# Kernel optimization log

Measured on AMD Instinct MI355X. Metric: run time of the kernel, lower is better.

The kernel has to match this reference:

```python
import jax, jax.numpy as jnp
import numpy as np

EMBED_DIM = 1024
NUM_HEADS = 16
HEAD_DIM = EMBED_DIM // NUM_HEADS
INV_SQRT_DIM = 1.0 / np.sqrt(EMBED_DIM).astype(np.float32)  # note: embed_dim, not head_dim


def setup_inputs() -> dict:
    key = jax.random.key(0)
    k1, k2 = jax.random.split(key)
    hidden_states = jax.random.normal(k1, (2, 2048, EMBED_DIM), dtype=jnp.float32)
    # nn.Linear(embed_dim, 3*embed_dim, bias=False); store as [in, out] so y = x @ w_qkv
    w_qkv = jax.random.normal(k2, (EMBED_DIM, 3 * EMBED_DIM), dtype=jnp.float32) * 0.02
    return {"hidden_states": hidden_states, "w_qkv": w_qkv}


def reference(hidden_states, w_qkv):
    b, s, _ = hidden_states.shape
    qkv = hidden_states @ w_qkv  # [b, s, 3*E]
    q, k, v = jnp.split(qkv, 3, axis=-1)

    def split_heads(x):  # [b, s, E] -> [b, h, s, d]
        return x.reshape(b, s, NUM_HEADS, HEAD_DIM).transpose(0, 2, 1, 3)

    q, k, v = split_heads(q), split_heads(k), split_heads(v)
    scores = jnp.einsum('bhqd,bhkd->bhqk', q, k) * INV_SQRT_DIM
    w = jax.nn.softmax(scores, axis=-1)
    out = jnp.einsum('bhqk,bhkd->bhqd', w, v)  # [b, h, s, d]
    return out.transpose(0, 2, 1, 3).reshape(b, s, EMBED_DIM)
```

## Files before the change

### kernel.cpp

```cpp
#include <hip/hip_runtime.h>
#include <stdint.h>


typedef __attribute__((ext_vector_type(8))) short v8s;
typedef __attribute__((ext_vector_type(4))) float v4f;
typedef __attribute__((ext_vector_type(16))) float f32x16;

__device__ __forceinline__ unsigned short bf16bits(float f) {
  union { float f; unsigned int u; } c; c.f = f;
  unsigned int u = c.u;
  unsigned int r = (u + 0x7fffu + ((u >> 16) & 1u)) >> 16;
  return (unsigned short)r;
}

__device__ __forceinline__ v4f mfma16(v8s a, v8s b, v4f c) {
  return __builtin_amdgcn_mfma_f32_16x16x32_bf16(a, b, c, 0, 0, 0);
}
__device__ __forceinline__ f32x16 mfma32(v8s a, v8s b, f32x16 c) {
  return __builtin_amdgcn_mfma_f32_32x32x16_bf16(a, b, c, 0, 0, 0);
}
__device__ __forceinline__ f32x16 zero16() {
  f32x16 z;
#pragma unroll
  for (int i = 0; i < 16; ++i) z[i] = 0.f;
  return z;
}
__device__ __forceinline__ unsigned int cvtpk(float lo, float hi) {
  unsigned int r;
  asm("v_cvt_pk_bf16_f32 %0, %1, %2" : "=v"(r) : "v"(lo), "v"(hi));
  return r;
}
__device__ __forceinline__ void pl32swap(unsigned int& a, unsigned int& b) {
  asm volatile("v_permlane32_swap_b32 %0, %1" : "+v"(a), "+v"(b));
}

#define GLD16(g, l) __builtin_amdgcn_global_load_lds( \
    (const __attribute__((address_space(1))) unsigned int*)(g), \
    (__attribute__((address_space(3))) unsigned int*)(l), 16, 0, 0)

__global__ __launch_bounds__(256) void cvt_x_kernel(const float4* __restrict__ x4,
                                                    ushort4* __restrict__ o4, int n4) {
  int i = blockIdx.x * 256 + threadIdx.x;
  if (i < n4) {
    float4 v = x4[i];
    ushort4 o;
    o.x = bf16bits(v.x); o.y = bf16bits(v.y); o.z = bf16bits(v.z); o.w = bf16bits(v.w);
    o4[i] = o;
  }
}

__global__ __launch_bounds__(256) void cvt_wT_kernel(const float* __restrict__ w,
                                                     unsigned short* __restrict__ wt) {
  __shared__ float t[32][33];
  int n0 = blockIdx.x * 32, k0 = blockIdx.y * 32;
  int tx = threadIdx.x & 31, ty = threadIdx.x >> 5;
  for (int i = 0; i < 4; ++i) {
    int kr = ty + i * 8;
    t[kr][tx] = w[(k0 + kr) * 3072 + n0 + tx];
  }
  __syncthreads();
  for (int i = 0; i < 4; ++i) {
    int nr = ty + i * 8;
    wt[(n0 + nr) * 1024 + k0 + tx] = bf16bits(t[tx][nr]);
  }
}

__global__ __launch_bounds__(256) void qkv_gemm(const unsigned short* __restrict__ A,
                                                const unsigned short* __restrict__ Bm,
                                                unsigned short* __restrict__ Cq,
                                                unsigned short* __restrict__ VTh) {
  __shared__ __align__(16) unsigned short S[24576];
  int bm = blockIdx.x, bn = blockIdx.y;
  int tid = threadIdx.x, lane = tid & 63, wave = tid >> 6;
  int wr = wave >> 1, wc = wave & 1;

  v4f acc[2][4];
  for (int i = 0; i < 2; ++i)
    for (int j = 0; j < 4; ++j) acc[i][j] = (v4f){0.f, 0.f, 0.f, 0.f};

  auto STAGE = [&](int hh, int kk) {
    unsigned short* As = S + hh * 12288;
    unsigned short* Bs = As + 4096;
    for (int i = 0; i < 2; ++i) {
      int e = i * 256 + tid;
      int row = e >> 3, cc = e & 7;
      int sc = cc ^ (row & 7);
      GLD16(A + (bm * 64 + row) * 1024 + kk + sc * 8,
            (char*)As + (i * 256 + wave * 64) * 16);
    }
    for (int i = 0; i < 4; ++i) {
      int e = i * 256 + tid;
      int row = e >> 3, cc = e & 7;
      int sc = cc ^ (row & 7);
      GLD16(Bm + (bn * 128 + row) * 1024 + kk + sc * 8,
            (char*)Bs + (i * 256 + wave * 64) * 16);
    }
  };
  auto COMPUTE = [&](int hh) {
    const unsigned short* As = S + hh * 12288;
    const unsigned short* Bs = As + 4096;
    for (int ks = 0; ks < 2; ++ks) {
      v8s af[2], bf[4];
      for (int rt = 0; rt < 2; ++rt) {
        int ra = wr * 32 + rt * 16 + (lane & 15);
        int ca = (ks * 4 + (lane >> 4)) ^ (ra & 7);
        af[rt] = *(const v8s*)&As[ra * 64 + ca * 8];
      }
      for (int ct = 0; ct < 4; ++ct) {
        int rb = wc * 64 + ct * 16 + (lane & 15);
        int cb = (ks * 4 + (lane >> 4)) ^ (rb & 7);
        bf[ct] = *(const v8s*)&Bs[rb * 64 + cb * 8];
      }
      for (int rt = 0; rt < 2; ++rt)
        for (int ct = 0; ct < 4; ++ct)
          acc[rt][ct] = mfma16(af[rt], bf[ct], acc[rt][ct]);
    }
  };

  STAGE(0, 0);
  __syncthreads();
  for (int kt = 0; kt < 15; ++kt) {
    STAGE((kt + 1) & 1, (kt + 1) * 64);
    COMPUTE(kt & 1);
    __syncthreads();
  }
  COMPUTE(1);
  __syncthreads();

  if (bn < 16) {
    float qs = (bn < 8) ? 0.0450842200f : 1.0f;
    for (int ct = 0; ct < 4; ++ct) {
      int col = wc * 64 + ct * 16 + (lane & 15);
      for (int rt = 0; rt < 2; ++rt)
        for (int j = 0; j < 4; ++j) {
          int m = wr * 32 + rt * 16 + ((lane >> 4) << 2) + j;
          S[m * 128 + (((col >> 3) ^ (m & 7)) << 3) + (col & 7)] =
              bf16bits(acc[rt][ct][j] * qs);
        }
    }
    __syncthreads();
    for (int i = 0; i < 4; ++i) {
      int c = i * 256 + tid;
      int m = c >> 4, c8 = c & 15;
      v8s v = *(const v8s*)&S[m * 128 + ((c8 ^ (m & 7)) << 3)];
      *(v8s*)&Cq[(size_t)(bm * 64 + m) * 2048 + bn * 128 + c8 * 8] = v;
    }
  } else {
    for (int ct = 0; ct < 4; ++ct) {
      int n = wc * 64 + ct * 16 + (lane & 15);
      for (int rt = 0; rt < 2; ++rt) {
        int m0 = wr * 32 + rt * 16 + ((lane >> 4) << 2);
        ushort4 p4;
        p4.x = bf16bits(acc[rt][ct][0]); p4.y = bf16bits(acc[rt][ct][1]);
        p4.z = bf16bits(acc[rt][ct][2]); p4.w = bf16bits(acc[rt][ct][3]);
        *(ushort4*)&S[n * 64 + (((m0 >> 3) ^ (n & 7)) << 3) + (m0 & 7)] = p4;
      }
    }
    __syncthreads();
    int b = bm >> 5, s0 = (bm & 31) * 64;
    for (int i = 0; i < 4; ++i) {
      int c = i * 256 + tid;
      int n = c >> 3, c8 = c & 7;
      v8s v = *(const v8s*)&S[n * 64 + ((c8 ^ (n & 7)) << 3)];
      int nn = bn * 128 + n - 2048;
      int head = nn >> 6, d = nn & 63;
      *(v8s*)&VTh[(size_t)((b * 16 + head) * 64 + d) * 2048 + s0 + c8 * 8] = v;
    }
  }
}

__global__ __launch_bounds__(256) void attn_kernel(const unsigned short* __restrict__ Cq,
                                                   const unsigned short* __restrict__ VTh,
                                                   float* __restrict__ out) {
  __shared__ __align__(16) unsigned short Qs[128 * 64];
  __shared__ __align__(16) unsigned short Ks[64 * 64];
  __shared__ __align__(16) unsigned short Vs[64 * 64];
  int tid = threadIdx.x, lane = tid & 63, wave = tid >> 6;
  int ln31 = lane & 31, h = lane >> 5;
  int wq = wave * 32;
  int flat = blockIdx.x + (blockIdx.y << 4);
  int swz = (flat & 7) * 64 + (flat >> 3);
  int qb = swz & 15, bh = swz >> 4;
  int b = bh >> 4, hH = bh & 15;

  const unsigned short* Qg = Cq + (size_t)(b * 2048 + qb * 128) * 2048 + hH * 64;
  const unsigned short* Kg = Cq + (size_t)(b * 2048) * 2048 + 1024 + hH * 64;
  const unsigned short* Vg = VTh + (size_t)bh * 64 * 2048;

  for (int i = 0; i < 4; ++i) {
    int e = i * 256 + tid;
    int row = e >> 3, cc = e & 7;
    int sc = cc ^ (row & 7);
    GLD16(Qg + (size_t)row * 2048 + sc * 8, (char*)Qs + (i * 256 + wave * 64) * 16);
  }
  __syncthreads();

  v8s qf[4];
#pragma unroll
  for (int ks = 0; ks < 4; ++ks) {
    int rq = wq + ln31;
    int cq = (ks * 2 + h) ^ (rq & 7);
    qf[ks] = *(const v8s*)&Qs[rq * 64 + cq * 8];
  }

  f32x16 acc0 = zero16(), acc1 = zero16();
  float rsum = 0.f;

  for (int kt = 0; kt < 32; ++kt) {
    __syncthreads();
    for (int i = 0; i < 2; ++i) {
      int e = i * 256 + tid;
      int row = e >> 3, cc = e & 7;
      int sc = cc ^ (row & 7);
      GLD16(Kg + (size_t)(kt * 64 + row) * 2048 + sc * 8,
            (char*)Ks + (i * 256 + wave * 64) * 16);
    }
    for (int i = 0; i < 2; ++i) {
      int e = i * 256 + tid;
      int row = e >> 3, cc = e & 7;
      int sc = cc ^ (row & 7);
      GLD16(Vg + row * 2048 + kt * 64 + sc * 8, (char*)Vs + (i * 256 + wave * 64) * 16);
    }
    __syncthreads();

    f32x16 s0 = zero16(), s1 = zero16();
#pragma unroll
    for (int ks = 0; ks < 4; ++ks) {
      int ck = (ks * 2 + h) ^ (ln31 & 7);
      v8s kf0 = *(const v8s*)&Ks[ln31 * 64 + ck * 8];
      v8s kf1 = *(const v8s*)&Ks[(32 + ln31) * 64 + ck * 8];
      s0 = mfma32(kf0, qf[ks], s0);
      s1 = mfma32(kf1, qf[ks], s1);
    }

#pragma unroll
    for (int mt = 0; mt < 2; ++mt) {
      const f32x16 st = mt ? s1 : s0;
      float p[16];
#pragma unroll
      for (int r = 0; r < 16; ++r) { p[r] = __builtin_amdgcn_exp2f(st[r]); rsum += p[r]; }
      unsigned int w0 = cvtpk(p[0], p[1]),  w1 = cvtpk(p[2], p[3]);
      unsigned int w2 = cvtpk(p[4], p[5]),  w3 = cvtpk(p[6], p[7]);
      unsigned int w4 = cvtpk(p[8], p[9]),  w5 = cvtpk(p[10], p[11]);
      unsigned int w6 = cvtpk(p[12], p[13]), w7 = cvtpk(p[14], p[15]);
      pl32swap(w0, w2); pl32swap(w1, w3);
      pl32swap(w4, w6); pl32swap(w5, w7);
      union { unsigned int u[4]; v8s v; } pa0, pa1;
      pa0.u[0] = w0; pa0.u[1] = w1; pa0.u[2] = w2; pa0.u[3] = w3;
      pa1.u[0] = w4; pa1.u[1] = w5; pa1.u[2] = w6; pa1.u[3] = w7;
#pragma unroll
      for (int s = 0; s < 2; ++s) {
        v8s pa = s ? pa1.v : pa0.v;
        int cb = mt * 4 + s * 2 + h;
        int rv0 = ln31, rv1 = 32 + ln31;
        v8s vb0 = *(const v8s*)&Vs[rv0 * 64 + ((cb ^ (rv0 & 7))) * 8];
        v8s vb1 = *(const v8s*)&Vs[rv1 * 64 + ((cb ^ (rv1 & 7))) * 8];
        acc0 = mfma32(pa, vb0, acc0);
        acc1 = mfma32(pa, vb1, acc1);
      }
    }
  }

  float rtot = rsum + __shfl_xor(rsum, 32, 64);
  float inv = 1.0f / rtot;

  int qbase = qb * 128 + wq;
#pragma unroll
  for (int r = 0; r < 16; ++r) {
    int qr = (r & 3) + 8 * (r >> 2) + 4 * h;
    float ivr = __shfl(inv, qr, 64);
    size_t o = (size_t)(b * 2048 + qbase + qr) * 1024 + hH * 64 + ln31;
    out[o] = acc0[r] * ivr;
    out[o + 32] = acc1[r] * ivr;
  }
}

extern "C" void kernel_launch(void* const* d_in, const int* in_sizes, int n_in,
                              void* d_out, int out_size, void* d_ws, size_t ws_size,
                              hipStream_t stream) {
  const float* x = (const float*)d_in[0];
  const float* w = (const float*)d_in[1];
  float* out = (float*)d_out;

  char* ws = (char*)d_ws;
  unsigned short* xb = (unsigned short*)ws;
  unsigned short* wT = (unsigned short*)(ws + 8388608);
  unsigned short* Cq = (unsigned short*)(ws + 14680064);
  unsigned short* VT = (unsigned short*)(ws + 31457280);

  cvt_x_kernel<<<4096, 256, 0, stream>>>((const float4*)x, (ushort4*)xb, 1048576);
  cvt_wT_kernel<<<dim3(96, 32), 256, 0, stream>>>(w, wT);
  qkv_gemm<<<dim3(64, 24), 256, 0, stream>>>(xb, wT, Cq, VT);
  attn_kernel<<<dim3(16, 32), 256, 0, stream>>>(Cq, VT, out);
}
```

Baseline: 156.2 us.

## Split attention KV loop across wave pairs and swizzle QKV GEMM block order

```diff
diff --git a/kernel.cpp b/kernel.cpp
--- a/kernel.cpp
+++ b/kernel.cpp
@@ -70,9 +70,11 @@
                                                 unsigned short* __restrict__ Cq,
                                                 unsigned short* __restrict__ VTh) {
   __shared__ __align__(16) unsigned short S[24576];
-  int bm = blockIdx.x, bn = blockIdx.y;
   int tid = threadIdx.x, lane = tid & 63, wave = tid >> 6;
   int wr = wave >> 1, wc = wave & 1;
+  int flat = blockIdx.x + blockIdx.y * 64;
+  int x = flat & 7, k = flat >> 3;
+  int bm = k & 63, bn = (k >> 6) * 8 + x;
 
   v4f acc[2][4];
   for (int i = 0; i < 2; ++i)
@@ -172,22 +174,22 @@
 __global__ __launch_bounds__(256) void attn_kernel(const unsigned short* __restrict__ Cq,
                                                    const unsigned short* __restrict__ VTh,
                                                    float* __restrict__ out) {
-  __shared__ __align__(16) unsigned short Qs[128 * 64];
-  __shared__ __align__(16) unsigned short Ks[64 * 64];
-  __shared__ __align__(16) unsigned short Vs[64 * 64];
+  __shared__ __align__(16) unsigned short Qs[64 * 64];
+  __shared__ __align__(16) unsigned short Ks[2][64 * 64];
+  __shared__ __align__(16) unsigned short Vs[2][64 * 64];
   int tid = threadIdx.x, lane = tid & 63, wave = tid >> 6;
   int ln31 = lane & 31, h = lane >> 5;
-  int wq = wave * 32;
-  int flat = blockIdx.x + (blockIdx.y << 4);
-  int swz = (flat & 7) * 64 + (flat >> 3);
-  int qb = swz & 15, bh = swz >> 4;
+  int qhalf = wave & 1, kpar = wave >> 1;
+  int flat = blockIdx.x + (blockIdx.y << 5);
+  int swz = (flat & 7) * 128 + (flat >> 3);
+  int qb = swz & 31, bh = swz >> 5;
   int b = bh >> 4, hH = bh & 15;
 
-  const unsigned short* Qg = Cq + (size_t)(b * 2048 + qb * 128) * 2048 + hH * 64;
+  const unsigned short* Qg = Cq + (size_t)(b * 2048 + qb * 64) * 2048 + hH * 64;
   const unsigned short* Kg = Cq + (size_t)(b * 2048) * 2048 + 1024 + hH * 64;
   const unsigned short* Vg = VTh + (size_t)bh * 64 * 2048;
 
-  for (int i = 0; i < 4; ++i) {
+  for (int i = 0; i < 2; ++i) {
     int e = i * 256 + tid;
     int row = e >> 3, cc = e & 7;
     int sc = cc ^ (row & 7);
@@ -198,7 +200,7 @@
   v8s qf[4];
 #pragma unroll
   for (int ks = 0; ks < 4; ++ks) {
-    int rq = wq + ln31;
+    int rq = qhalf * 32 + ln31;
     int cq = (ks * 2 + h) ^ (rq & 7);
     qf[ks] = *(const v8s*)&Qs[rq * 64 + cq * 8];
   }
@@ -206,29 +208,32 @@
   f32x16 acc0 = zero16(), acc1 = zero16();
   float rsum = 0.f;
 
-  for (int kt = 0; kt < 32; ++kt) {
+  for (int t = 0; t < 16; ++t) {
     __syncthreads();
     for (int i = 0; i < 2; ++i) {
       int e = i * 256 + tid;
       int row = e >> 3, cc = e & 7;
       int sc = cc ^ (row & 7);
-      GLD16(Kg + (size_t)(kt * 64 + row) * 2048 + sc * 8,
-            (char*)Ks + (i * 256 + wave * 64) * 16);
-    }
-    for (int i = 0; i < 2; ++i) {
-      int e = i * 256 + tid;
-      int row = e >> 3, cc = e & 7;
-      int sc = cc ^ (row & 7);
-      GLD16(Vg + row * 2048 + kt * 64 + sc * 8, (char*)Vs + (i * 256 + wave * 64) * 16);
-    }
-    __syncthreads();
+      GLD16(Kg + (size_t)((2 * t) * 64 + row) * 2048 + sc * 8,
+            (char*)Ks[0] + (i * 256 + wave * 64) * 16);
+      GLD16(Kg + (size_t)((2 * t + 1) * 64 + row) * 2048 + sc * 8,
+            (char*)Ks[1] + (i * 256 + wave * 64) * 16);
+      GLD16(Vg + row * 2048 + (2 * t) * 64 + sc * 8,
+            (char*)Vs[0] + (i * 256 + wave * 64) * 16);
+      GLD16(Vg + row * 2048 + (2 * t + 1) * 64 + sc * 8,
+            (char*)Vs[1] + (i * 256 + wave * 64) * 16);
+    }
+    __syncthreads();
+
+    const unsigned short* Ksp = Ks[kpar];
+    const unsigned short* Vsp = Vs[kpar];
 
     f32x16 s0 = zero16(), s1 = zero16();
 #pragma unroll
     for (int ks = 0; ks < 4; ++ks) {
       int ck = (ks * 2 + h) ^ (ln31 & 7);
-      v8s kf0 = *(const v8s*)&Ks[ln31 * 64 + ck * 8];
-      v8s kf1 = *(const v8s*)&Ks[(32 + ln31) * 64 + ck * 8];
+      v8s kf0 = *(const v8s*)&Ksp[ln31 * 64 + ck * 8];
+      v8s kf1 = *(const v8s*)&Ksp[(32 + ln31) * 64 + ck * 8];
       s0 = mfma32(kf0, qf[ks], s0);
       s1 = mfma32(kf1, qf[ks], s1);
     }
@@ -253,25 +258,48 @@
         v8s pa = s ? pa1.v : pa0.v;
         int cb = mt * 4 + s * 2 + h;
         int rv0 = ln31, rv1 = 32 + ln31;
-        v8s vb0 = *(const v8s*)&Vs[rv0 * 64 + ((cb ^ (rv0 & 7))) * 8];
-        v8s vb1 = *(const v8s*)&Vs[rv1 * 64 + ((cb ^ (rv1 & 7))) * 8];
+        v8s vb0 = *(const v8s*)&Vsp[rv0 * 64 + ((cb ^ (rv0 & 7))) * 8];
+        v8s vb1 = *(const v8s*)&Vsp[rv1 * 64 + ((cb ^ (rv1 & 7))) * 8];
         acc0 = mfma32(pa, vb0, acc0);
         acc1 = mfma32(pa, vb1, acc1);
       }
     }
   }
 
-  float rtot = rsum + __shfl_xor(rsum, 32, 64);
-  float inv = 1.0f / rtot;
-
-  int qbase = qb * 128 + wq;
-#pragma unroll
-  for (int r = 0; r < 16; ++r) {
-    int qr = (r & 3) + 8 * (r >> 2) + 4 * h;
-    float ivr = __shfl(inv, qr, 64);
-    size_t o = (size_t)(b * 2048 + qbase + qr) * 1024 + hH * 64 + ln31;
-    out[o] = acc0[r] * ivr;
-    out[o + 32] = acc1[r] * ivr;
+  __syncthreads();
+  float* accx = (float*)&Ks[0][0];
+  float* rsx = (float*)&Vs[0][0];
+  if (kpar == 1) {
+    int r = qhalf;
+#pragma unroll
+    for (int j = 0; j < 16; ++j) {
+      accx[r * 2048 + j * 64 + lane] = acc0[j];
+      accx[r * 2048 + (16 + j) * 64 + lane] = acc1[j];
+    }
+    rsx[r * 64 + lane] = rsum;
+  }
+  __syncthreads();
+  if (kpar == 0) {
+    int r = qhalf;
+#pragma unroll
+    for (int j = 0; j < 16; ++j) {
+      acc0[j] += accx[r * 2048 + j * 64 + lane];
+      acc1[j] += accx[r * 2048 + (16 + j) * 64 + lane];
+    }
+    rsum += rsx[r * 64 + lane];
+
+    float rtot = rsum + __shfl_xor(rsum, 32, 64);
+    float inv = 1.0f / rtot;
+
+    int qbase = qb * 64 + qhalf * 32;
+#pragma unroll
+    for (int r2 = 0; r2 < 16; ++r2) {
+      int qr = (r2 & 3) + 8 * (r2 >> 2) + 4 * h;
+      float ivr = __shfl(inv, qr, 64);
+      size_t o = (size_t)(b * 2048 + qbase + qr) * 1024 + hH * 64 + ln31;
+      out[o] = acc0[r2] * ivr;
+      out[o + 32] = acc1[r2] * ivr;
+    }
   }
 }
 
@@ -291,5 +319,5 @@
   cvt_x_kernel<<<4096, 256, 0, stream>>>((const float4*)x, (ushort4*)xb, 1048576);
   cvt_wT_kernel<<<dim3(96, 32), 256, 0, stream>>>(w, wT);
   qkv_gemm<<<dim3(64, 24), 256, 0, stream>>>(xb, wT, Cq, VT);
-  attn_kernel<<<dim3(16, 32), 256, 0, stream>>>(Cq, VT, out);
-}
+  attn_kernel<<<dim3(32, 32), 256, 0, stream>>>(Cq, VT, out);
+}
```

After: 165.8 us. +6.2%, slower.
